# Optimization experiments

Measured on AMD Instinct MI355X. Metric: run time of the kernel, lower is better.

The kernel has to match this reference:

```python
import jax, jax.numpy as jnp
import numpy as np

B, T, N, D, H, NMASK = 8192, 2, 40, 64, 1, 3
EPS = 1e-5


def setup_inputs() -> dict:
    key = jax.random.key(0)
    ks = jax.random.split(key, 12)
    F = T * N * 2 * D  # flattened feature size fed to BatchNorm1d
    return {
        "x": jax.random.normal(ks[0], (B, N, D), jnp.float32),
        "masker": jax.random.uniform(ks[1], (T, NMASK, N, N), jnp.float32, -0.27, 0.27),  # xavier-like
        "ln_gamma": jnp.ones((N,), jnp.float32),
        "ln_beta": jnp.zeros((N,), jnp.float32),
        "gnn_w": jax.random.normal(ks[2], (1, T, H, 2 * D, D), jnp.float32) * 0.05,
        "gnn_b": jax.random.normal(ks[3], (T, H, N, D), jnp.float32) * 0.05,
        "bn_gamma": jnp.ones((H, F), jnp.float32),
        "bn_beta": jnp.zeros((H, F), jnp.float32),
        "bn_mean": jax.random.normal(ks[4], (H, F), jnp.float32) * 0.1,
        "bn_var": jax.random.uniform(ks[5], (H, F), jnp.float32, 0.5, 1.5),
        "gate_w": jax.random.normal(ks[6], (N * D, N), jnp.float32) * 0.02,
        "gate_b": jnp.zeros((N,), jnp.float32),
    }


def reference(x, masker, ln_gamma, ln_beta, gnn_w, gnn_b, bn_gamma, bn_beta, bn_mean, bn_var, gate_w, gate_b):
    b = x.shape[0]
    # broadcast input to towers: (B, T, N, D)
    h = jnp.broadcast_to(x[:, None], (b, T, N, D))
    # adjacency from product of mask matrices: (T, N, N)
    adj = jax.nn.relu(jnp.prod(masker, axis=1))
    mask = (adj != 0).astype(x.dtype)
    # LayerNorm(num_fields) applied on transposed adj == normalize over rows (axis -2)
    mu = adj.mean(axis=-2, keepdims=True)
    var = adj.var(axis=-2, keepdims=True)
    ln = (adj - mu) / jnp.sqrt(var + EPS) * ln_gamma[:, None] + ln_beta[:, None]
    x_masked = ln + (1.0 - mask) * (-1e9) + jnp.eye(N, dtype=x.dtype)
    # softmax over rows (dim=1 of (T,N,N)) then re-mask
    A = jax.nn.softmax(x_masked, axis=1) * mask  # (T, N, N)
    for idx in range(H):
        # nei[b,t,n,d] = sum_m h[b,t,m,d] * A[t,m,n]
        nei = jnp.einsum('btmd,tmn->btnd', h, A)
        hc = jnp.concatenate([h, nei], axis=-1)  # (B,T,N,2D)
        flat = hc.reshape(b, -1)
        flat = (flat - bn_mean[idx]) / jnp.sqrt(bn_var[idx] + EPS) * bn_gamma[idx] + bn_beta[idx]
        hc = flat.reshape(b, T, N, 2 * D)
        # per-tower transform: (B,T,N,2D) x (T,2D,D) -> (B,T,N,D)
        h = jnp.einsum('btnf,tfd->btnd', hc, gnn_w[0, :, idx]) + gnn_b[:, idx]
    # attention pooling over fields
    logits = h.reshape(b, T, N * D) @ gate_w + gate_b  # (B,T,N)
    w = jax.nn.softmax(logits, axis=2)
    return jnp.sum(h * w[..., None], axis=2)  # (B, T, D)
```

## Files before the change

kernel.cpp:

```cpp
#include <hip/hip_runtime.h>
#include <hip/hip_bf16.h>
#include <stdint.h>

typedef float v4f __attribute__((ext_vector_type(4)));
typedef short v8s __attribute__((ext_vector_type(8)));

#define NB 40

__device__ __forceinline__ unsigned short f2b(float f) {
  __hip_bfloat16 h = __float2bfloat16(f);
  unsigned short u;
  __builtin_memcpy(&u, &h, 2);
  return u;
}
__device__ __forceinline__ unsigned pk2(float lo, float hi) {
  __hip_bfloat162 h = __float22bfloat162_rn(make_float2(lo, hi));
  unsigned u;
  __builtin_memcpy(&u, &h, 4);
  return u;
}
__device__ __forceinline__ float b2f16(unsigned short h) {
  return __uint_as_float(((unsigned)h) << 16);
}
__device__ __forceinline__ float blo(unsigned u) { return __uint_as_float(u << 16); }
__device__ __forceinline__ float bhi(unsigned u) { return __uint_as_float(u & 0xFFFF0000u); }


__global__ __launch_bounds__(256) void prep(
    const float* __restrict__ masker,
    const float* __restrict__ ln_gamma, const float* __restrict__ ln_beta,
    const float* __restrict__ gnn_w, const float* __restrict__ gnn_b,
    const float* __restrict__ bn_gamma, const float* __restrict__ bn_beta,
    const float* __restrict__ bn_mean, const float* __restrict__ bn_var,
    const float* __restrict__ gate_w,
    unsigned short* __restrict__ A1pk, unsigned short* __restrict__ W2pk,
    unsigned short* __restrict__ Gpk, float* __restrict__ s1,
    float* __restrict__ sNT, float* __restrict__ bias2T)
{
  const int tid = threadIdx.x;
  if (blockIdx.x == 0) {
    __shared__ float AtL[2 * NB * NB];
    const int w = tid >> 6, lane = tid & 63;
    #pragma unroll 1
    for (int it = 0; it < 20; ++it) {
      const int c = it * 4 + w;
      const int t = c / NB, n = c % NB;
      const int m = lane;
      float adj = 0.f;
      if (m < NB) {
        float p = masker[((t*3+0)*NB+m)*NB+n]
                * masker[((t*3+1)*NB+m)*NB+n]
                * masker[((t*3+2)*NB+m)*NB+n];
        adj = p > 0.f ? p : 0.f;
      }
      float s = adj;
      #pragma unroll
      for (int d = 1; d < 64; d <<= 1) s += __shfl_xor(s, d);
      const float mu = s * (1.f/NB);
      const float dv = (m < NB) ? adj - mu : 0.f;
      float v2 = dv * dv;
      #pragma unroll
      for (int d = 1; d < 64; d <<= 1) v2 += __shfl_xor(v2, d);
      const float inv = rsqrtf(v2 * (1.f/NB) + 1e-5f);
      float val = -3.0e38f;
      if (m < NB) {
        float lnv = dv * inv * ln_gamma[m] + ln_beta[m];
        val = lnv + (adj != 0.f ? 0.f : -1e9f) + (m == n ? 1.f : 0.f);
      }
      float mx = val;
      #pragma unroll
      for (int d = 1; d < 64; d <<= 1) mx = fmaxf(mx, __shfl_xor(mx, d));
      const float e = (m < NB) ? __expf(val - mx) : 0.f;
      float es = e;
      #pragma unroll
      for (int d = 1; d < 64; d <<= 1) es += __shfl_xor(es, d);
      if (m < NB)
        AtL[(t*NB+n)*NB + m] = (adj != 0.f) ? e / es : 0.f;
    }
    __syncthreads();
    for (int e = tid; e < 6144; e += 256) {
      int frag = e >> 9, rem = e & 511, lane2 = rem >> 3, jj = rem & 7;
      int t = frag / 6, r2 = frag % 6, nt = r2 >> 1, ks = r2 & 1;
      int n = nt*16 + (lane2 & 15);
      int m = ks*32 + (lane2 >> 4)*8 + jj;
      A1pk[e] = f2b((n < NB && m < NB) ? AtL[(t*NB+n)*NB+m] : 0.f);
    }
  } else {
    const int gid = (blockIdx.x - 1) * 256 + tid, gsz = 63 * 256;
    for (int e = gid; e < 16384; e += gsz) {
      int frag = e >> 9, rem = e & 511, lane = rem >> 3, jj = rem & 7;
      int t = frag >> 4, ks = (frag >> 2) & 3, dt = frag & 3;
      int f = ks*32 + (lane >> 4)*8 + jj, d = dt*16 + (lane & 15);
      W2pk[e] = f2b(gnn_w[t*8192 + f*64 + d]);
    }
    for (int e = gid; e < 122880; e += gsz) {
      int frag = e >> 9, rem = e & 511, lane = rem >> 3, jj = rem & 7;
      int kt = frag / 3, jt = frag % 3;
      int fl = kt*32 + (lane >> 4)*8 + jj, j = jt*16 + (lane & 15);
      Gpk[e] = f2b(j < NB ? gate_w[fl*NB + j] : 0.f);
    }
    for (int e = gid; e < 5120; e += gsz) {
      int t = e / 2560, n = (e % 2560) / 64, d = e & 63;
      int F = (t*NB + n)*128 + d;
      s1[e] = bn_gamma[F] * rsqrtf(bn_var[F] + 1e-5f);
    }
    for (int e = gid; e < 5120; e += gsz) {
      int t = e / 2560, d = (e % 2560) / 40, n = e % 40;
      int F = (t*NB + n)*128 + 64 + d;
      sNT[e] = bn_gamma[F] * rsqrtf(bn_var[F] + 1e-5f);
    }
    for (int e4 = gid; e4 < 20480; e4 += gsz) {
      int e = e4 >> 2, part = e4 & 3;
      int t = e / 2560, d = (e % 2560) / 40, n = e % 40;
      float acc = (part == 0) ? gnn_b[(t*NB + n)*64 + d] : 0.f;
      int Fb = (t*NB + n)*128;
      int f0 = part * 32;
      for (int f = f0; f < f0 + 32; ++f) {
        float s = bn_gamma[Fb+f] * rsqrtf(bn_var[Fb+f] + 1e-5f);
        float o = bn_beta[Fb+f] - bn_mean[Fb+f] * s;
        acc += o * gnn_w[t*8192 + f*64 + d];
      }
      acc += __shfl_xor(acc, 1);
      acc += __shfl_xor(acc, 2);
      if (part == 0) bias2T[e] = acc;
    }
  }
}

__global__ __launch_bounds__(256) void kernelM(
    const float* __restrict__ x,
    const unsigned short* __restrict__ A1pk, const unsigned short* __restrict__ W2pk,
    const unsigned short* __restrict__ Gpk, const float* __restrict__ s1,
    const float* __restrict__ sNT, const float* __restrict__ bias2T,
    const float* __restrict__ gate_b, float* __restrict__ out)
{
  __shared__ __align__(16) unsigned short hc[160 * 136];
  __shared__ float pj[16 * 48];

  const int tid = threadIdx.x;
  const int lane = tid & 63;
  const int w = tid >> 6;
  const int l = lane & 15, q = lane >> 4;
  const int t = blockIdx.x & 1;
  const int b0 = (blockIdx.x >> 1) * 4;
  unsigned* hcU = (unsigned*)hc;
  unsigned short* hL = hc;

  uint4 xr[5];
  #pragma unroll
  for (int it = 0; it < 5; ++it) {
    const int c = it * 256 + tid, row = c >> 3, dp8 = c & 7;
    const float* xp = x + (size_t)b0 * 2560 + row * 64 + dp8 * 8;
    const float4 f0 = *(const float4*)xp;
    const float4 f1 = *(const float4*)(xp + 4);
    xr[it] = make_uint4(pk2(f0.x, f0.y), pk2(f0.z, f0.w),
                        pk2(f1.x, f1.y), pk2(f1.z, f1.w));
  }
  if (tid < 12) hcU[5120 + tid] = 0u;
  #pragma unroll
  for (int it = 0; it < 5; ++it) {
    const int c = it * 256 + tid, row = c >> 3, dp8 = c & 7;
    const int bq = row / NB, n = row - bq * NB;
    unsigned short* base = hc + (bq * 64 + dp8 * 8) * NB + n;
    const unsigned uu0 = xr[it].x, uu1 = xr[it].y, uu2 = xr[it].z, uu3 = xr[it].w;
    base[0*NB] = (unsigned short)(uu0 & 0xFFFF);
    base[1*NB] = (unsigned short)(uu0 >> 16);
    base[2*NB] = (unsigned short)(uu1 & 0xFFFF);
    base[3*NB] = (unsigned short)(uu1 >> 16);
    base[4*NB] = (unsigned short)(uu2 & 0xFFFF);
    base[5*NB] = (unsigned short)(uu2 >> 16);
    base[6*NB] = (unsigned short)(uu3 & 0xFFFF);
    base[7*NB] = (unsigned short)(uu3 >> 16);
  }
  __syncthreads();
  v8s b1[4][2];
  #pragma unroll
  for (int i = 0; i < 4; ++i)
    #pragma unroll
    for (int ks = 0; ks < 2; ++ks)
      b1[i][ks] = *(const v8s*)(hc + ((w * 4 + i) * 16 + l) * NB + ks * 32 + q * 8);
  __syncthreads();

  v8s a1[3][2], w2[4];
  #pragma unroll
  for (int nt = 0; nt < 3; ++nt)
    #pragma unroll
    for (int ks = 0; ks < 2; ++ks)
      a1[nt][ks] = *(const v8s*)(A1pk + (((t*3 + nt)*2 + ks) << 9) + lane*8);
  #pragma unroll
  for (int ks = 0; ks < 4; ++ks)
    w2[ks] = *(const v8s*)(W2pk + (((t*4 + ks)*4 + w) << 9) + lane*8);

  #pragma unroll
  for (int it = 0; it < 5; ++it) {
    const int c = it*256 + tid;
    const int row = c >> 3, dp8 = c & 7;
    const uint4 xv = xr[it];
    const int n = row % NB;
    const float4 sA = *(const float4*)(s1 + (t*NB + n)*64 + dp8*8);
    const float4 sB = *(const float4*)(s1 + (t*NB + n)*64 + dp8*8 + 4);
    uint4 p;
    p.x = pk2(blo(xv.x)*sA.x, bhi(xv.x)*sA.y);
    p.y = pk2(blo(xv.y)*sA.z, bhi(xv.y)*sA.w);
    p.z = pk2(blo(xv.z)*sB.x, bhi(xv.z)*sB.y);
    p.w = pk2(blo(xv.w)*sB.z, bhi(xv.w)*sB.w);
    *(uint4*)(hcU + row*68 + dp8*4) = p;
  }
  #pragma unroll
  for (int i = 0; i < 4; ++i) {
    const int R = (w*4+i)*16 + l;
    const int bb = R >> 6, d = R & 63;
    #pragma unroll
    for (int nt = 0; nt < 3; ++nt) {
      v4f acc = {0.f, 0.f, 0.f, 0.f};
      acc = __builtin_amdgcn_mfma_f32_16x16x32_bf16(a1[nt][0], b1[i][0], acc, 0, 0, 0);
      acc = __builtin_amdgcn_mfma_f32_16x16x32_bf16(a1[nt][1], b1[i][1], acc, 0, 0, 0);
      const float4 sv = *(const float4*)(sNT + (t*64+d)*40 + nt*16 + q*4);
      #pragma unroll
      for (int r = 0; r < 4; ++r) {
        int n = nt*16 + q*4 + r;
        if (n < NB) hc[(bb*NB + n)*136 + 64 + d] = f2b(acc[r]*sv[r]);
      }
    }
  }
  __syncthreads();
  unsigned pkr0[10], pkr1[10];
  #pragma unroll
  for (int mt = 0; mt < 10; ++mt) {
    v4f acc = {0.f, 0.f, 0.f, 0.f};
    #pragma unroll
    for (int ks = 0; ks < 4; ++ks) {
      v8s af = *(const v8s*)(hc + (mt*16 + l)*136 + ks*32 + q*8);
      acc = __builtin_amdgcn_mfma_f32_16x16x32_bf16(af, w2[ks], acc, 0, 0, 0);
    }
    const int d = w*16 + l;
    const int G = mt*16 + q*4;
    const int bb = G / NB, n0 = G - bb*NB;
    const float4 bv = *(const float4*)(bias2T + (t*64+d)*40 + n0);
    pkr0[mt] = pk2(acc[0] + bv.x, acc[1] + bv.y);
    pkr1[mt] = pk2(acc[2] + bv.z, acc[3] + bv.w);
  }
  __syncthreads();
  #pragma unroll
  for (int mt = 0; mt < 10; ++mt) {
    const int d = w*16 + l;
    const int G = mt*16 + q*4;
    const int bb = G / NB, n0 = G - bb*NB;
    hL[bb*2568 + (n0+0)*64 + d] = (unsigned short)(pkr0[mt] & 0xFFFF);
    hL[bb*2568 + (n0+1)*64 + d] = (unsigned short)(pkr0[mt] >> 16);
    hL[bb*2568 + (n0+2)*64 + d] = (unsigned short)(pkr1[mt] & 0xFFFF);
    hL[bb*2568 + (n0+3)*64 + d] = (unsigned short)(pkr1[mt] >> 16);
  }
  __syncthreads();
  v4f ac0 = {0,0,0,0}, ac1 = {0,0,0,0}, ac2 = {0,0,0,0};
  {
    v8s pg0[2], pg1[2], pg2[2], pbf[2];
    #pragma unroll
    for (int s = 0; s < 2; ++s) {
      const int kt = w + s*4;
      pg0[s] = *(const v8s*)(Gpk + ((kt*3+0) << 9) + lane*8);
      pg1[s] = *(const v8s*)(Gpk + ((kt*3+1) << 9) + lane*8);
      pg2[s] = *(const v8s*)(Gpk + ((kt*3+2) << 9) + lane*8);
      pbf[s] = *(const v8s*)(hL + (l & 3)*2568 + kt*32 + q*8);
    }
    #pragma unroll
    for (int i = 0; i < 20; ++i) {
      const int cur = i & 1;
      const v8s G0 = pg0[cur], G1 = pg1[cur], G2 = pg2[cur], BF = pbf[cur];
      if (i < 18) {
        const int ktn = w + (i+2)*4;
        pg0[cur] = *(const v8s*)(Gpk + ((ktn*3+0) << 9) + lane*8);
        pg1[cur] = *(const v8s*)(Gpk + ((ktn*3+1) << 9) + lane*8);
        pg2[cur] = *(const v8s*)(Gpk + ((ktn*3+2) << 9) + lane*8);
        pbf[cur] = *(const v8s*)(hL + (l & 3)*2568 + ktn*32 + q*8);
      }
      ac0 = __builtin_amdgcn_mfma_f32_16x16x32_bf16(G0, BF, ac0, 0, 0, 0);
      ac1 = __builtin_amdgcn_mfma_f32_16x16x32_bf16(G1, BF, ac1, 0, 0, 0);
      ac2 = __builtin_amdgcn_mfma_f32_16x16x32_bf16(G2, BF, ac2, 0, 0, 0);
    }
  }
  if (l < 4) {
    #pragma unroll
    for (int r = 0; r < 4; ++r) {
      pj[(w*4 + l)*48 +  0 + q*4 + r] = ac0[r];
      pj[(w*4 + l)*48 + 16 + q*4 + r] = ac1[r];
      pj[(w*4 + l)*48 + 32 + q*4 + r] = ac2[r];
    }
  }
  __syncthreads();
  {
    float v = -3.0e38f;
    if (lane < NB) {
      v = gate_b[lane];
      #pragma unroll
      for (int ww = 0; ww < 4; ++ww) v += pj[(ww*4 + w)*48 + lane];
    }
    float mx = v;
    #pragma unroll
    for (int m = 1; m < 64; m <<= 1) mx = fmaxf(mx, __shfl_xor(mx, m));
    float e = (lane < NB) ? __expf(v - mx) : 0.f;
    float es = e;
    #pragma unroll
    for (int m = 1; m < 64; m <<= 1) es += __shfl_xor(es, m);
    const float wgt = e / es;
    float accp = 0.f;
    #pragma unroll 8
    for (int n = 0; n < NB; ++n)
      accp += b2f16(hL[w*2568 + n*64 + lane]) * __shfl(wgt, n);
    out[((size_t)(b0 + w)*2 + t)*64 + lane] = accp;
  }
}

extern "C" void kernel_launch(void* const* d_in, const int* in_sizes, int n_in,
                              void* d_out, int out_size, void* d_ws, size_t ws_size,
                              hipStream_t stream) {
  const float* x        = (const float*)d_in[0];
  const float* masker   = (const float*)d_in[1];
  const float* ln_gamma = (const float*)d_in[2];
  const float* ln_beta  = (const float*)d_in[3];
  const float* gnn_w    = (const float*)d_in[4];
  const float* gnn_b    = (const float*)d_in[5];
  const float* bn_gamma = (const float*)d_in[6];
  const float* bn_beta  = (const float*)d_in[7];
  const float* bn_mean  = (const float*)d_in[8];
  const float* bn_var   = (const float*)d_in[9];
  const float* gate_w   = (const float*)d_in[10];
  const float* gate_b   = (const float*)d_in[11];
  float* out = (float*)d_out;

  char* ws = (char*)d_ws;
  unsigned short* A1pk   = (unsigned short*)(ws + 0);
  unsigned short* W2pk   = (unsigned short*)(ws + 12288);
  unsigned short* Gpk    = (unsigned short*)(ws + 45056);
  float*          s1     = (float*)(ws + 290816);
  float*          sNT    = (float*)(ws + 311296);
  float*          bias2T = (float*)(ws + 331904);

  prep<<<64, 256, 0, stream>>>(masker, ln_gamma, ln_beta, gnn_w, gnn_b,
                               bn_gamma, bn_beta, bn_mean, bn_var, gate_w,
                               A1pk, W2pk, Gpk, s1, sNT, bias2T);
  kernelM<<<4096, 256, 0, stream>>>(x, A1pk, W2pk, Gpk,
                                    s1, sNT, bias2T, gate_b, out);
}
```

Before: 238.4 us.

## Build scaled-x MFMA operands from global loads instead of staging in LDS

The BN-scaled x half of the concatenated features is no longer written to shared memory. Each wave re-reads x and s1 from global memory and packs the bf16 A-fragments directly in registers for the second GEMM. This shrinks the shared buffer from 160x136 to 160x72 shorts and drops the register array that held x across the phases, which should raise occupancy and cut LDS traffic. In exchange x is read from global twice per block (relying on cache hits) and more conversion arithmetic runs inside the MFMA loop.

```diff
diff --git a/kernel.cpp b/kernel.cpp
--- a/kernel.cpp
+++ b/kernel.cpp
@@ -4,6 +4,7 @@
 
 typedef float v4f __attribute__((ext_vector_type(4)));
 typedef short v8s __attribute__((ext_vector_type(8)));
+typedef union { v8s v; unsigned u[4]; } v8u;
 
 #define NB 40
 
@@ -134,7 +135,7 @@
     const float* __restrict__ sNT, const float* __restrict__ bias2T,
     const float* __restrict__ gate_b, float* __restrict__ out)
 {
-  __shared__ __align__(16) unsigned short hc[160 * 136];
+  __shared__ __align__(16) unsigned short hc[11520];
   __shared__ float pj[16 * 48];
 
   const int tid = threadIdx.x;
@@ -146,32 +147,26 @@
   unsigned* hcU = (unsigned*)hc;
   unsigned short* hL = hc;
 
-  uint4 xr[5];
+  const float* xblk = x + (size_t)b0 * 2560;
+
   #pragma unroll
   for (int it = 0; it < 5; ++it) {
     const int c = it * 256 + tid, row = c >> 3, dp8 = c & 7;
-    const float* xp = x + (size_t)b0 * 2560 + row * 64 + dp8 * 8;
+    const float* xp = xblk + row * 64 + dp8 * 8;
     const float4 f0 = *(const float4*)xp;
     const float4 f1 = *(const float4*)(xp + 4);
-    xr[it] = make_uint4(pk2(f0.x, f0.y), pk2(f0.z, f0.w),
-                        pk2(f1.x, f1.y), pk2(f1.z, f1.w));
-  }
-  if (tid < 12) hcU[5120 + tid] = 0u;
-  #pragma unroll
-  for (int it = 0; it < 5; ++it) {
-    const int c = it * 256 + tid, row = c >> 3, dp8 = c & 7;
     const int bq = row / NB, n = row - bq * NB;
     unsigned short* base = hc + (bq * 64 + dp8 * 8) * NB + n;
-    const unsigned uu0 = xr[it].x, uu1 = xr[it].y, uu2 = xr[it].z, uu3 = xr[it].w;
-    base[0*NB] = (unsigned short)(uu0 & 0xFFFF);
-    base[1*NB] = (unsigned short)(uu0 >> 16);
-    base[2*NB] = (unsigned short)(uu1 & 0xFFFF);
-    base[3*NB] = (unsigned short)(uu1 >> 16);
-    base[4*NB] = (unsigned short)(uu2 & 0xFFFF);
-    base[5*NB] = (unsigned short)(uu2 >> 16);
-    base[6*NB] = (unsigned short)(uu3 & 0xFFFF);
-    base[7*NB] = (unsigned short)(uu3 >> 16);
-  }
+    base[0*NB] = f2b(f0.x);
+    base[1*NB] = f2b(f0.y);
+    base[2*NB] = f2b(f0.z);
+    base[3*NB] = f2b(f0.w);
+    base[4*NB] = f2b(f1.x);
+    base[5*NB] = f2b(f1.y);
+    base[6*NB] = f2b(f1.z);
+    base[7*NB] = f2b(f1.w);
+  }
+  if (tid < 12) hcU[5120 + tid] = 0u;
   __syncthreads();
   v8s b1[4][2];
   #pragma unroll
@@ -181,64 +176,73 @@
       b1[i][ks] = *(const v8s*)(hc + ((w * 4 + i) * 16 + l) * NB + ks * 32 + q * 8);
   __syncthreads();
 
-  v8s a1[3][2], w2[4];
-  #pragma unroll
-  for (int nt = 0; nt < 3; ++nt)
-    #pragma unroll
-    for (int ks = 0; ks < 2; ++ks)
-      a1[nt][ks] = *(const v8s*)(A1pk + (((t*3 + nt)*2 + ks) << 9) + lane*8);
-  #pragma unroll
-  for (int ks = 0; ks < 4; ++ks)
-    w2[ks] = *(const v8s*)(W2pk + (((t*4 + ks)*4 + w) << 9) + lane*8);
-
-  #pragma unroll
-  for (int it = 0; it < 5; ++it) {
-    const int c = it*256 + tid;
-    const int row = c >> 3, dp8 = c & 7;
-    const uint4 xv = xr[it];
-    const int n = row % NB;
-    const float4 sA = *(const float4*)(s1 + (t*NB + n)*64 + dp8*8);
-    const float4 sB = *(const float4*)(s1 + (t*NB + n)*64 + dp8*8 + 4);
-    uint4 p;
-    p.x = pk2(blo(xv.x)*sA.x, bhi(xv.x)*sA.y);
-    p.y = pk2(blo(xv.y)*sA.z, bhi(xv.y)*sA.w);
-    p.z = pk2(blo(xv.z)*sB.x, bhi(xv.z)*sB.y);
-    p.w = pk2(blo(xv.w)*sB.z, bhi(xv.w)*sB.w);
-    *(uint4*)(hcU + row*68 + dp8*4) = p;
-  }
-  #pragma unroll
-  for (int i = 0; i < 4; ++i) {
-    const int R = (w*4+i)*16 + l;
-    const int bb = R >> 6, d = R & 63;
-    #pragma unroll
-    for (int nt = 0; nt < 3; ++nt) {
+  {
+    v8s a1[3][2];
+    #pragma unroll
+    for (int nt = 0; nt < 3; ++nt)
+      #pragma unroll
+      for (int ks = 0; ks < 2; ++ks)
+        a1[nt][ks] = *(const v8s*)(A1pk + (((t*3 + nt)*2 + ks) << 9) + lane*8);
+    #pragma unroll
+    for (int i = 0; i < 4; ++i) {
+      const int R = (w*4+i)*16 + l;
+      const int bb = R >> 6, d = R & 63;
+      #pragma unroll
+      for (int nt = 0; nt < 3; ++nt) {
+        v4f acc = {0.f, 0.f, 0.f, 0.f};
+        acc = __builtin_amdgcn_mfma_f32_16x16x32_bf16(a1[nt][0], b1[i][0], acc, 0, 0, 0);
+        acc = __builtin_amdgcn_mfma_f32_16x16x32_bf16(a1[nt][1], b1[i][1], acc, 0, 0, 0);
+        const float4 sv = *(const float4*)(sNT + (t*64+d)*40 + nt*16 + q*4);
+        #pragma unroll
+        for (int r = 0; r < 4; ++r) {
+          int n = nt*16 + q*4 + r;
+          if (n < NB) hc[(bb*NB + n)*72 + d] = f2b(acc[r]*sv[r]);
+        }
+      }
+    }
+  }
+  __syncthreads();
+  unsigned pkr0[10], pkr1[10];
+  {
+    v8s w2[4];
+    #pragma unroll
+    for (int ks = 0; ks < 4; ++ks)
+      w2[ks] = *(const v8s*)(W2pk + (((t*4 + ks)*4 + w) << 9) + lane*8);
+    #pragma unroll
+    for (int mt = 0; mt < 10; ++mt) {
+      const int row = mt*16 + l;
+      int n = (mt*16) % NB + l;
+      if (n >= NB) n -= NB;
+      const float* xp = xblk + row * 64;
+      const float* sp = s1 + (t*NB + n) * 64;
+      v8s af[4];
+      #pragma unroll
+      for (int ks = 0; ks < 2; ++ks) {
+        const int f0 = ks*32 + q*8;
+        const float4 xa = *(const float4*)(xp + f0);
+        const float4 xc = *(const float4*)(xp + f0 + 4);
+        const float4 sa = *(const float4*)(sp + f0);
+        const float4 sc = *(const float4*)(sp + f0 + 4);
+        v8u uu;
+        uu.u[0] = pk2(xa.x*sa.x, xa.y*sa.y);
+        uu.u[1] = pk2(xa.z*sa.z, xa.w*sa.w);
+        uu.u[2] = pk2(xc.x*sc.x, xc.y*sc.y);
+        uu.u[3] = pk2(xc.z*sc.z, xc.w*sc.w);
+        af[ks] = uu.v;
+      }
+      af[2] = *(const v8s*)(hc + row*72 + q*8);
+      af[3] = *(const v8s*)(hc + row*72 + 32 + q*8);
       v4f acc = {0.f, 0.f, 0.f, 0.f};
-      acc = __builtin_amdgcn_mfma_f32_16x16x32_bf16(a1[nt][0], b1[i][0], acc, 0, 0, 0);
-      acc = __builtin_amdgcn_mfma_f32_16x16x32_bf16(a1[nt][1], b1[i][1], acc, 0, 0, 0);
-      const float4 sv = *(const float4*)(sNT + (t*64+d)*40 + nt*16 + q*4);
-      #pragma unroll
-      for (int r = 0; r < 4; ++r) {
-        int n = nt*16 + q*4 + r;
-        if (n < NB) hc[(bb*NB + n)*136 + 64 + d] = f2b(acc[r]*sv[r]);
-      }
-    }
-  }
-  __syncthreads();
-  unsigned pkr0[10], pkr1[10];
-  #pragma unroll
-  for (int mt = 0; mt < 10; ++mt) {
-    v4f acc = {0.f, 0.f, 0.f, 0.f};
-    #pragma unroll
-    for (int ks = 0; ks < 4; ++ks) {
-      v8s af = *(const v8s*)(hc + (mt*16 + l)*136 + ks*32 + q*8);
-      acc = __builtin_amdgcn_mfma_f32_16x16x32_bf16(af, w2[ks], acc, 0, 0, 0);
-    }
-    const int d = w*16 + l;
-    const int G = mt*16 + q*4;
-    const int bb = G / NB, n0 = G - bb*NB;
-    const float4 bv = *(const float4*)(bias2T + (t*64+d)*40 + n0);
-    pkr0[mt] = pk2(acc[0] + bv.x, acc[1] + bv.y);
-    pkr1[mt] = pk2(acc[2] + bv.z, acc[3] + bv.w);
+      #pragma unroll
+      for (int ks = 0; ks < 4; ++ks)
+        acc = __builtin_amdgcn_mfma_f32_16x16x32_bf16(af[ks], w2[ks], acc, 0, 0, 0);
+      const int d = w*16 + l;
+      const int G = mt*16 + q*4;
+      const int bb = G / NB, n0 = G - bb*NB;
+      const float4 bv = *(const float4*)(bias2T + (t*64+d)*40 + n0);
+      pkr0[mt] = pk2(acc[0] + bv.x, acc[1] + bv.y);
+      pkr1[mt] = pk2(acc[2] + bv.z, acc[3] + bv.w);
+    }
   }
   __syncthreads();
   #pragma unroll
```

New measurement: 325.9 us. +36.7%, slower.

## Pad transposed LDS layouts to 44-wide rows with packed 32-bit stores

Applied to the files above, without the earlier changes.

The transposed x tile in LDS now uses 22-dword rows, a 44-element pitch. Neighbouring lanes exchange halves via shuffle so each LDS write is a packed 32-bit word instead of eight 16-bit stores. The post-transform h buffer is stored d-major with a 44-element pitch using 64-bit stores, and the gate weight packing is reordered and zero-padded to match. This makes the gate GEMM run 22 k-steps over padded columns and lets the pooling loop read vector pairs. The aim is fewer LDS store instructions and fewer bank conflicts, at the cost of extra MFMA work on padding and a larger packed gate-weight buffer.

```diff
diff --git a/kernel.cpp b/kernel.cpp
--- a/kernel.cpp
+++ b/kernel.cpp
@@ -4,8 +4,10 @@
 
 typedef float v4f __attribute__((ext_vector_type(4)));
 typedef short v8s __attribute__((ext_vector_type(8)));
+typedef union { v8s v; unsigned u[4]; } v8u;
 
 #define NB 40
+#define BSTR 2848
 
 __device__ __forceinline__ unsigned short f2b(float f) {
   __hip_bfloat16 h = __float2bfloat16(f);
@@ -93,11 +95,13 @@
       int f = ks*32 + (lane >> 4)*8 + jj, d = dt*16 + (lane & 15);
       W2pk[e] = f2b(gnn_w[t*8192 + f*64 + d]);
     }
-    for (int e = gid; e < 122880; e += gsz) {
+    for (int e = gid; e < 135168; e += gsz) {
       int frag = e >> 9, rem = e & 511, lane = rem >> 3, jj = rem & 7;
       int kt = frag / 3, jt = frag % 3;
-      int fl = kt*32 + (lane >> 4)*8 + jj, j = jt*16 + (lane & 15);
-      Gpk[e] = f2b(j < NB ? gate_w[fl*NB + j] : 0.f);
+      int flp = kt*32 + (lane >> 4)*8 + jj;
+      int dd = flp / 44, nn = flp - dd*44;
+      int j = jt*16 + (lane & 15);
+      Gpk[e] = f2b((j < NB && nn < NB) ? gate_w[(nn*64 + dd)*NB + j] : 0.f);
     }
     for (int e = gid; e < 5120; e += gsz) {
       int t = e / 2560, n = (e % 2560) / 64, d = e & 63;
@@ -156,29 +160,42 @@
     xr[it] = make_uint4(pk2(f0.x, f0.y), pk2(f0.z, f0.w),
                         pk2(f1.x, f1.y), pk2(f1.z, f1.w));
   }
-  if (tid < 12) hcU[5120 + tid] = 0u;
-  #pragma unroll
-  for (int it = 0; it < 5; ++it) {
-    const int c = it * 256 + tid, row = c >> 3, dp8 = c & 7;
-    const int bq = row / NB, n = row - bq * NB;
-    unsigned short* base = hc + (bq * 64 + dp8 * 8) * NB + n;
-    const unsigned uu0 = xr[it].x, uu1 = xr[it].y, uu2 = xr[it].z, uu3 = xr[it].w;
-    base[0*NB] = (unsigned short)(uu0 & 0xFFFF);
-    base[1*NB] = (unsigned short)(uu0 >> 16);
-    base[2*NB] = (unsigned short)(uu1 & 0xFFFF);
-    base[3*NB] = (unsigned short)(uu1 >> 16);
-    base[4*NB] = (unsigned short)(uu2 & 0xFFFF);
-    base[5*NB] = (unsigned short)(uu2 >> 16);
-    base[6*NB] = (unsigned short)(uu3 & 0xFFFF);
-    base[7*NB] = (unsigned short)(uu3 >> 16);
+  for (int k = tid; k < 544; k += 256)
+    hcU[(k < 512) ? ((k >> 1) * 22 + 20 + (k & 1)) : (5632 + (k - 512))] = 0u;
+  {
+    const bool wr = (lane & 8) == 0;
+    #pragma unroll
+    for (int it = 0; it < 5; ++it) {
+      const int c = it * 256 + tid, row = c >> 3, dp8 = c & 7;
+      const int bq = row / NB, nn = row - bq * NB;
+      const int pp = nn >> 1;
+      const unsigned ua[4] = {xr[it].x, xr[it].y, xr[it].z, xr[it].w};
+      #pragma unroll
+      for (int cx = 0; cx < 4; ++cx) {
+        const unsigned ub = __shfl(ua[cx], lane | 8);
+        if (wr) {
+          const int R0 = bq * 64 + dp8 * 8 + cx * 2;
+          hcU[ R0      * 22 + pp] = (ua[cx] & 0xFFFFu) | (ub << 16);
+          hcU[(R0 + 1) * 22 + pp] = (ua[cx] >> 16) | (ub & 0xFFFF0000u);
+        }
+      }
+    }
   }
   __syncthreads();
   v8s b1[4][2];
   #pragma unroll
-  for (int i = 0; i < 4; ++i)
-    #pragma unroll
-    for (int ks = 0; ks < 2; ++ks)
-      b1[i][ks] = *(const v8s*)(hc + ((w * 4 + i) * 16 + l) * NB + ks * 32 + q * 8);
+  for (int i = 0; i < 4; ++i) {
+    const int R = (w * 4 + i) * 16 + l;
+    #pragma unroll
+    for (int ks = 0; ks < 2; ++ks) {
+      const unsigned* p = hcU + R * 22 + ks * 16 + q * 4;
+      const uint2 e0 = *(const uint2*)p;
+      const uint2 e1 = *(const uint2*)(p + 2);
+      v8u uu;
+      uu.u[0] = e0.x; uu.u[1] = e0.y; uu.u[2] = e1.x; uu.u[3] = e1.y;
+      b1[i][ks] = uu.v;
+    }
+  }
   __syncthreads();
 
   v8s a1[3][2], w2[4];
@@ -246,14 +263,18 @@
     const int d = w*16 + l;
     const int G = mt*16 + q*4;
     const int bb = G / NB, n0 = G - bb*NB;
-    hL[bb*2568 + (n0+0)*64 + d] = (unsigned short)(pkr0[mt] & 0xFFFF);
-    hL[bb*2568 + (n0+1)*64 + d] = (unsigned short)(pkr0[mt] >> 16);
-    hL[bb*2568 + (n0+2)*64 + d] = (unsigned short)(pkr1[mt] & 0xFFFF);
-    hL[bb*2568 + (n0+3)*64 + d] = (unsigned short)(pkr1[mt] >> 16);
+    uint2 pr; pr.x = pkr0[mt]; pr.y = pkr1[mt];
+    *(uint2*)(hL + bb*BSTR + d*44 + n0) = pr;
+  }
+  {
+    const int bb = tid >> 6, d = tid & 63;
+    uint2 z; z.x = 0u; z.y = 0u;
+    *(uint2*)(hL + bb*BSTR + d*44 + 40) = z;
   }
   __syncthreads();
   v4f ac0 = {0,0,0,0}, ac1 = {0,0,0,0}, ac2 = {0,0,0,0};
   {
+    const unsigned short* hb = hL + (l & 3)*BSTR + q*8;
     v8s pg0[2], pg1[2], pg2[2], pbf[2];
     #pragma unroll
     for (int s = 0; s < 2; ++s) {
@@ -261,18 +282,18 @@
       pg0[s] = *(const v8s*)(Gpk + ((kt*3+0) << 9) + lane*8);
       pg1[s] = *(const v8s*)(Gpk + ((kt*3+1) << 9) + lane*8);
       pg2[s] = *(const v8s*)(Gpk + ((kt*3+2) << 9) + lane*8);
-      pbf[s] = *(const v8s*)(hL + (l & 3)*2568 + kt*32 + q*8);
-    }
-    #pragma unroll
-    for (int i = 0; i < 20; ++i) {
+      pbf[s] = *(const v8s*)(hb + kt*32);
+    }
+    #pragma unroll
+    for (int i = 0; i < 22; ++i) {
       const int cur = i & 1;
       const v8s G0 = pg0[cur], G1 = pg1[cur], G2 = pg2[cur], BF = pbf[cur];
-      if (i < 18) {
+      if (i < 20) {
         const int ktn = w + (i+2)*4;
         pg0[cur] = *(const v8s*)(Gpk + ((ktn*3+0) << 9) + lane*8);
         pg1[cur] = *(const v8s*)(Gpk + ((ktn*3+1) << 9) + lane*8);
         pg2[cur] = *(const v8s*)(Gpk + ((ktn*3+2) << 9) + lane*8);
-        pbf[cur] = *(const v8s*)(hL + (l & 3)*2568 + ktn*32 + q*8);
+        pbf[cur] = *(const v8s*)(hb + ktn*32);
       }
       ac0 = __builtin_amdgcn_mfma_f32_16x16x32_bf16(G0, BF, ac0, 0, 0, 0);
       ac1 = __builtin_amdgcn_mfma_f32_16x16x32_bf16(G1, BF, ac1, 0, 0, 0);
@@ -304,9 +325,15 @@
     for (int m = 1; m < 64; m <<= 1) es += __shfl_xor(es, m);
     const float wgt = e / es;
     float accp = 0.f;
-    #pragma unroll 8
-    for (int n = 0; n < NB; ++n)
-      accp += b2f16(hL[w*2568 + n*64 + lane]) * __shfl(wgt, n);
+    const unsigned short* hp = hL + w*BSTR + lane*44;
+    #pragma unroll
+    for (int k = 0; k < 10; ++k) {
+      const uint2 rr = *(const uint2*)(hp + k*4);
+      accp += blo(rr.x) * __shfl(wgt, k*4 + 0);
+      accp += bhi(rr.x) * __shfl(wgt, k*4 + 1);
+      accp += blo(rr.y) * __shfl(wgt, k*4 + 2);
+      accp += bhi(rr.y) * __shfl(wgt, k*4 + 3);
+    }
     out[((size_t)(b0 + w)*2 + t)*64 + lane] = accp;
   }
 }
@@ -332,9 +359,9 @@
   unsigned short* A1pk   = (unsigned short*)(ws + 0);
   unsigned short* W2pk   = (unsigned short*)(ws + 12288);
   unsigned short* Gpk    = (unsigned short*)(ws + 45056);
-  float*          s1     = (float*)(ws + 290816);
-  float*          sNT    = (float*)(ws + 311296);
-  float*          bias2T = (float*)(ws + 331904);
+  float*          s1     = (float*)(ws + 315392);
+  float*          sNT    = (float*)(ws + 335872);
+  float*          bias2T = (float*)(ws + 356480);
 
   prep<<<64, 256, 0, stream>>>(masker, ln_gamma, ln_beta, gnn_w, gnn_b,
                                bn_gamma, bn_beta, bn_mean, bn_var, gate_w,
```

Result: slower. 245.4 us (+3.0%).
